# Kernel tuning notes

Measured on AMD Instinct MI355X. Metric: run time of the kernel, lower is better.

The kernel has to match this reference:

```python
import jax, jax.numpy as jnp
import numpy as np

N_FFT = 1024
HOP = 256
CACHE = N_FFT - 1  # causal left padding
EPS = 1e-12
BATCH = 16
SAMPLES = HOP * 2048


def _make_weight():
    # DFT basis modulated by a periodic Hann window (torch.hann_window default).
    n = np.arange(N_FFT, dtype=np.float32)
    k = np.arange(N_FFT // 2 + 1, dtype=np.float32)[:, None]
    ang = (-2.0 * np.pi / N_FFT) * k * n[None, :]
    win = 0.5 * (1.0 - np.cos(2.0 * np.pi * n / N_FFT))
    w = np.concatenate([np.cos(ang), np.sin(ang)], axis=0) * win  # [2*(N//2+1), N_FFT]
    return jnp.asarray(w, dtype=jnp.float32)[:, None, :]  # [O, I=1, K]


def setup_inputs() -> dict:
    key = jax.random.key(0)
    x = jax.random.normal(key, (BATCH, SAMPLES), dtype=jnp.float32)
    return {"x": x, "weight": _make_weight()}


def reference(x, weight):
    if x.ndim == 2:
        x = x[:, None, :]  # [B, 1, T]
    # causal constant (zero) padding on the left
    x = jnp.pad(x, ((0, 0), (0, 0), (CACHE, 0)))
    # strided conv against the fixed DFT basis: [B, 2*(N//2+1), L]
    y = jax.lax.conv_general_dilated(
        x, weight, window_strides=(HOP,), padding='VALID',
        dimension_numbers=('NCH', 'OIH', 'NCH'))
    B, C, T = y.shape
    y = y.reshape(B, 2, C // 2, T)  # real/imag split
    mag = jnp.sqrt(jnp.clip(jnp.sum(y * y, axis=1), EPS, None))  # [B, N//2+1, L]
    return mag
```

## Files before the change

### kernel.cpp

```cpp
#include <hip/hip_runtime.h>
#include <stdint.h>

#define SAMPLES   524288
#define BATCH     16
#define T_FRAMES  2048
#define K_FFT     1024
#define HOPSZ     256
#define CACHEPAD  1023
#define NCH       513
#define XROW      525312

typedef __bf16          bf16x8 __attribute__((ext_vector_type(8)));
typedef float           f32x4  __attribute__((ext_vector_type(4)));
typedef unsigned short  u16x8  __attribute__((ext_vector_type(8)));

__device__ __forceinline__ unsigned short f2bf(float f) {
    union { float f; unsigned u; } v; v.f = f;
    unsigned r = v.u + 0x7fffu + ((v.u >> 16) & 1u);
    return (unsigned short)(r >> 16);
}

__global__ void prep(const float* __restrict__ x, const float* __restrict__ wsrc,
                     unsigned short* __restrict__ Xb, unsigned short* __restrict__ Wb) {
    const int bid = blockIdx.x;
    const int tid = threadIdx.x;
    if (bid < 512) {
        int gid = bid * 256 + tid;
        int m   = gid >> 7;
        int kc  = (gid & 127) << 3;
        int q = m >> 5, h = (m >> 4) & 1, r = m & 15;
        int bin  = q * 16 + r;
        int srow = (h == 0) ? bin : (bin == 0 ? 512 : NCH + bin);
        const float* s = wsrc + (long long)srow * K_FFT + kc;
        f32x4 a = *(const f32x4*)s;
        f32x4 c = *(const f32x4*)(s + 4);
        union { u16x8 v; unsigned short e[8]; } o;
        o.e[0]=f2bf(a[0]); o.e[1]=f2bf(a[1]); o.e[2]=f2bf(a[2]); o.e[3]=f2bf(a[3]);
        o.e[4]=f2bf(c[0]); o.e[5]=f2bf(c[1]); o.e[6]=f2bf(c[2]); o.e[7]=f2bf(c[3]);
        *(u16x8*)(Wb + (long long)m * K_FFT + kc) = o.v;
    } else {
        int id  = bid - 512;
        int bat = id >> 8;
        int bx  = id & 255;
        unsigned short* xbo = Xb + (long long)bat * XROW;
        if (bx == 0) {
            for (int j = tid; j < CACHEPAD; j += 256) xbo[j] = 0;
            if (tid == 0) xbo[XROW - 1] = 0;
        }
        int i0 = (bx * 256 + tid) * 8;
        const float* xb = x + (long long)bat * SAMPLES;
        f32x4 a = *(const f32x4*)&xb[i0];
        f32x4 c = *(const f32x4*)&xb[i0 + 4];
        unsigned short* dst = xbo + CACHEPAD + i0;
        dst[0]=f2bf(a[0]); dst[1]=f2bf(a[1]); dst[2]=f2bf(a[2]); dst[3]=f2bf(a[3]);
        dst[4]=f2bf(c[0]); dst[5]=f2bf(c[1]); dst[6]=f2bf(c[2]); dst[7]=f2bf(c[3]);
    }
}

__device__ __forceinline__ void gll16(const unsigned short* g, unsigned short* s) {
    __builtin_amdgcn_global_load_lds(
        (const __attribute__((address_space(1))) void*)g,
        (__attribute__((address_space(3))) void*)s,
        16, 0, 0);
}

#define MFMA(a,b,c) __builtin_amdgcn_mfma_f32_16x16x32_bf16((a),(b),(c),0,0,0)

__global__ __launch_bounds__(512, 2)
void stft_gemm(const unsigned short* __restrict__ Xb,
               const unsigned short* __restrict__ Wb,
               float* __restrict__ out) {
    __shared__ unsigned short S[65536];

    const int id  = blockIdx.x;
    const int xcd = id & 7;
    const int u   = id >> 3;
    const int nt  = u >> 4;
    const int ft  = (xcd << 4) | (u & 15);
    const int b   = ft >> 3;
    const int t0  = (ft & 7) << 8;

    const int tid = threadIdx.x;
    const int l   = tid & 63;
    const int wv  = tid >> 6;
    const int ln  = l & 15;
    const int qd  = l >> 4;
    const int wm  = wv & 1;
    const int wn  = wv >> 1;

    const int sr0 = wv * 32 + (l >> 2);
    const int sr1 = sr0 + 16;
    const int sch = ((l & 3) ^ ((l >> 3) & 3)) * 8;
    const unsigned short* wA0 = Wb + (long long)(nt * 256 + sr0) * K_FFT + sch;
    const unsigned short* wA1 = Wb + (long long)(nt * 256 + sr1) * K_FFT + sch;
    const unsigned short* xbase = Xb + (long long)b * XROW;
    const unsigned short* fB0 = xbase + (t0 + sr0) * HOPSZ + sch;
    const unsigned short* fB1 = xbase + (t0 + sr1) * HOPSZ + sch;
    const int d0 = wv * 1024;
    const int d1 = d0 + 512;

    const int cx   = (qd ^ ((ln >> 1) & 3)) * 8;
    const int aoff = (wm * 128 + ln) * 32 + cx;
    const int boff = (wn * 64  + ln) * 32 + cx;

    f32x4 acc[8][4];
    #pragma unroll
    for (int i = 0; i < 8; ++i)
        #pragma unroll
        for (int jn = 0; jn < 4; ++jn) acc[i][jn] = (f32x4){0.f,0.f,0.f,0.f};

    gll16(wA0 +  0, S +     0 + d0);  gll16(wA1 +  0, S +     0 + d1);
    gll16(fB0 +  0, S +  8192 + d0);  gll16(fB1 +  0, S +  8192 + d1);
    gll16(wA0 + 32, S + 16384 + d0);  gll16(wA1 + 32, S + 16384 + d1);
    gll16(fB0 + 32, S + 24576 + d0);  gll16(fB1 + 32, S + 24576 + d1);
    gll16(wA0 + 64, S + 32768 + d0);  gll16(wA1 + 64, S + 32768 + d1);
    gll16(fB0 + 64, S + 40960 + d0);  gll16(fB1 + 64, S + 40960 + d1);
    asm volatile("s_waitcnt vmcnt(4)" ::: "memory");
    __builtin_amdgcn_s_barrier();

    #pragma unroll 1
    for (int j = 0; j < 16; ++j) {
        const int bb  = (j & 1) << 15;
        const int bb1 = bb ^ 32768;
        const int kA  = j * 64 + 96;
        const int kB  = j * 64 + 128;

        bf16x8 av[8];
        if (j < 15) { gll16(wA0 + kA, S + bb1 + 16384 + d0);
                      gll16(wA1 + kA, S + bb1 + 16384 + d1); }
        {
            const unsigned short* pA = S + bb + aoff;
            const unsigned short* pB = S + bb + 8192 + boff;
            #pragma unroll
            for (int i = 0; i < 8; ++i) av[i] = *(const bf16x8*)(pA + i * 512);
            bf16x8 b0 = *(const bf16x8*)(pB);
            bf16x8 b1 = *(const bf16x8*)(pB + 512);
            __builtin_amdgcn_s_barrier();
            __builtin_amdgcn_s_setprio(1);
            #pragma unroll
            for (int i = 0; i < 8; ++i) {
                acc[i][0] = MFMA(av[i], b0, acc[i][0]);
                acc[i][1] = MFMA(av[i], b1, acc[i][1]);
            }
            __builtin_amdgcn_s_setprio(0);
            __builtin_amdgcn_s_barrier();
        }
        if (j < 15) { gll16(fB0 + kA, S + bb1 + 24576 + d0);
                      gll16(fB1 + kA, S + bb1 + 24576 + d1); }
        {
            const unsigned short* pB = S + bb + 8192 + boff;
            bf16x8 b2 = *(const bf16x8*)(pB + 1024);
            bf16x8 b3 = *(const bf16x8*)(pB + 1536);
            __builtin_amdgcn_s_barrier();
            __builtin_amdgcn_s_setprio(1);
            #pragma unroll
            for (int i = 0; i < 8; ++i) {
                acc[i][2] = MFMA(av[i], b2, acc[i][2]);
                acc[i][3] = MFMA(av[i], b3, acc[i][3]);
            }
            __builtin_amdgcn_s_setprio(0);
            __builtin_amdgcn_s_barrier();
        }
        if (j < 14) { gll16(wA0 + kB, S + bb + d0);
                      gll16(wA1 + kB, S + bb + d1); }
        {
            const unsigned short* pA = S + bb + 16384 + aoff;
            const unsigned short* pB = S + bb + 24576 + boff;
            #pragma unroll
            for (int i = 0; i < 8; ++i) av[i] = *(const bf16x8*)(pA + i * 512);
            bf16x8 b0 = *(const bf16x8*)(pB);
            bf16x8 b1 = *(const bf16x8*)(pB + 512);
            __builtin_amdgcn_s_barrier();
            __builtin_amdgcn_s_setprio(1);
            #pragma unroll
            for (int i = 0; i < 8; ++i) {
                acc[i][0] = MFMA(av[i], b0, acc[i][0]);
                acc[i][1] = MFMA(av[i], b1, acc[i][1]);
            }
            __builtin_amdgcn_s_setprio(0);
            __builtin_amdgcn_s_barrier();
        }
        if (j < 14) { gll16(fB0 + kB, S + bb + 8192 + d0);
                      gll16(fB1 + kB, S + bb + 8192 + d1); }
        {
            const unsigned short* pB = S + bb + 24576 + boff;
            bf16x8 b2 = *(const bf16x8*)(pB + 1024);
            bf16x8 b3 = *(const bf16x8*)(pB + 1536);
            __builtin_amdgcn_s_barrier();
            __builtin_amdgcn_s_setprio(1);
            #pragma unroll
            for (int i = 0; i < 8; ++i) {
                acc[i][2] = MFMA(av[i], b2, acc[i][2]);
                acc[i][3] = MFMA(av[i], b3, acc[i][3]);
            }
            __builtin_amdgcn_s_setprio(0);
            if (j == 14) { asm volatile("s_waitcnt vmcnt(0)" ::: "memory"); }
            else         { asm volatile("s_waitcnt vmcnt(4)" ::: "memory"); }
            __builtin_amdgcn_s_barrier();
        }
    }

    float* outb = out + (long long)b * (NCH * T_FRAMES);
    const int tb = t0 + wn * 64 + ln;
    const int binbase = (nt * 8 + wm * 4) * 16 + qd * 4;
    #pragma unroll
    for (int p = 0; p < 4; ++p) {
        #pragma unroll
        for (int jn = 0; jn < 4; ++jn) {
            const int t = tb + jn * 16;
            #pragma unroll
            for (int r = 0; r < 4; ++r) {
                float re = acc[2 * p][jn][r];
                float im = acc[2 * p + 1][jn][r];
                int bin = binbase + p * 16 + r;
                if (bin == 0) {
                    outb[t] = sqrtf(fmaxf(re * re, 1e-12f));
                    outb[(long long)512 * T_FRAMES + t] = sqrtf(fmaxf(im * im, 1e-12f));
                } else {
                    outb[(long long)bin * T_FRAMES + t] =
                        sqrtf(fmaxf(re * re + im * im, 1e-12f));
                }
            }
        }
    }
}

extern "C" void kernel_launch(void* const* d_in, const int* in_sizes, int n_in,
                              void* d_out, int out_size, void* d_ws, size_t ws_size,
                              hipStream_t stream) {
    const float* x  = (const float*)d_in[0];
    const float* wt = (const float*)d_in[1];
    float* out = (float*)d_out;

    unsigned short* Xb = (unsigned short*)d_ws;
    unsigned short* Wb = (unsigned short*)((char*)d_ws + (size_t)33554432);

    prep<<<4608, 256, 0, stream>>>(x, wt, Xb, Wb);
    stft_gemm<<<512, 512, 0, stream>>>(Xb, Wb, out);
}
```

Measured before the change: 154.3 us.

## Process two frame tiles per block with continuous pipelined K loop

Each block now computes two consecutive 256-frame tiles for the same bin tile. The two K loops are merged into one 32-step double-buffered loop, so prefetch of the second tile starts before the first tile's epilogue. Accumulators are written out and cleared mid-loop. The grid drops from 512 to 256 blocks. The goal is to amortise pipeline ramp-up and drain and the block launch cost, but there are fewer blocks to fill the CUs and the epilogue now sits inside the main loop.

```diff
diff --git a/kernel.cpp b/kernel.cpp
--- a/kernel.cpp
+++ b/kernel.cpp
@@ -75,10 +75,10 @@
     const int id  = blockIdx.x;
     const int xcd = id & 7;
     const int u   = id >> 3;
-    const int nt  = u >> 4;
-    const int ft  = (xcd << 4) | (u & 15);
-    const int b   = ft >> 3;
-    const int t0  = (ft & 7) << 8;
+    const int nt  = u >> 3;
+    const int fp  = (xcd << 3) | (u & 7);
+    const int b   = fp >> 2;
+    const int offF = (fp & 3) << 9;
 
     const int tid = threadIdx.x;
     const int l   = tid & 63;
@@ -94,8 +94,8 @@
     const unsigned short* wA0 = Wb + (long long)(nt * 256 + sr0) * K_FFT + sch;
     const unsigned short* wA1 = Wb + (long long)(nt * 256 + sr1) * K_FFT + sch;
     const unsigned short* xbase = Xb + (long long)b * XROW;
-    const unsigned short* fB0 = xbase + (t0 + sr0) * HOPSZ + sch;
-    const unsigned short* fB1 = xbase + (t0 + sr1) * HOPSZ + sch;
+    const unsigned short* fB0 = xbase + (offF + sr0) * HOPSZ + sch;
+    const unsigned short* fB1 = xbase + (offF + sr1) * HOPSZ + sch;
     const int d0 = wv * 1024;
     const int d1 = d0 + 512;
 
@@ -118,15 +118,22 @@
     asm volatile("s_waitcnt vmcnt(4)" ::: "memory");
     __builtin_amdgcn_s_barrier();
 
+    float* outb = out + (long long)b * (NCH * T_FRAMES);
+    const int binbase = (nt * 8 + wm * 4) * 16 + qd * 4;
+
     #pragma unroll 1
-    for (int j = 0; j < 16; ++j) {
+    for (int j = 0; j < 32; ++j) {
         const int bb  = (j & 1) << 15;
         const int bb1 = bb ^ 32768;
-        const int kA  = j * 64 + 96;
-        const int kB  = j * 64 + 128;
+        const int s1  = j + 1;
+        const int s2  = j + 2;
+        const int kA  = ((s1 & 15) << 6) + 32;
+        const int kB  = (s2 & 15) << 6;
+        const int ho1 = (s1 & 16) << 12;
+        const int ho2 = (s2 & 16) << 12;
 
         bf16x8 av[8];
-        if (j < 15) { gll16(wA0 + kA, S + bb1 + 16384 + d0);
+        if (j < 31) { gll16(wA0 + kA, S + bb1 + 16384 + d0);
                       gll16(wA1 + kA, S + bb1 + 16384 + d1); }
         {
             const unsigned short* pA = S + bb + aoff;
@@ -145,8 +152,8 @@
             __builtin_amdgcn_s_setprio(0);
             __builtin_amdgcn_s_barrier();
         }
-        if (j < 15) { gll16(fB0 + kA, S + bb1 + 24576 + d0);
-                      gll16(fB1 + kA, S + bb1 + 24576 + d1); }
+        if (j < 31) { gll16(fB0 + ho1 + kA, S + bb1 + 24576 + d0);
+                      gll16(fB1 + ho1 + kA, S + bb1 + 24576 + d1); }
         {
             const unsigned short* pB = S + bb + 8192 + boff;
             bf16x8 b2 = *(const bf16x8*)(pB + 1024);
@@ -161,7 +168,7 @@
             __builtin_amdgcn_s_setprio(0);
             __builtin_amdgcn_s_barrier();
         }
-        if (j < 14) { gll16(wA0 + kB, S + bb + d0);
+        if (j < 30) { gll16(wA0 + kB, S + bb + d0);
                       gll16(wA1 + kB, S + bb + d1); }
         {
             const unsigned short* pA = S + bb + 16384 + aoff;
@@ -180,8 +187,8 @@
             __builtin_amdgcn_s_setprio(0);
             __builtin_amdgcn_s_barrier();
         }
-        if (j < 14) { gll16(fB0 + kB, S + bb + 8192 + d0);
-                      gll16(fB1 + kB, S + bb + 8192 + d1); }
+        if (j < 30) { gll16(fB0 + ho2 + kB, S + bb + 8192 + d0);
+                      gll16(fB1 + ho2 + kB, S + bb + 8192 + d1); }
         {
             const unsigned short* pB = S + bb + 24576 + boff;
             bf16x8 b2 = *(const bf16x8*)(pB + 1024);
@@ -194,31 +201,59 @@
                 acc[i][3] = MFMA(av[i], b3, acc[i][3]);
             }
             __builtin_amdgcn_s_setprio(0);
-            if (j == 14) { asm volatile("s_waitcnt vmcnt(0)" ::: "memory"); }
+            if (j == 30) { asm volatile("s_waitcnt vmcnt(0)" ::: "memory"); }
             else         { asm volatile("s_waitcnt vmcnt(4)" ::: "memory"); }
             __builtin_amdgcn_s_barrier();
         }
+
+        if (j == 15) {
+            const int tb = offF + wn * 64 + ln;
+            #pragma unroll
+            for (int p = 0; p < 4; ++p) {
+                #pragma unroll
+                for (int jn = 0; jn < 4; ++jn) {
+                    const int t = tb + jn * 16;
+                    #pragma unroll
+                    for (int r = 0; r < 4; ++r) {
+                        float re = acc[2 * p][jn][r];
+                        float im = acc[2 * p + 1][jn][r];
+                        int bin = binbase + p * 16 + r;
+                        if (bin == 0) {
+                            outb[t] = sqrtf(fmaxf(re * re, 1e-12f));
+                            outb[(long long)512 * T_FRAMES + t] = sqrtf(fmaxf(im * im, 1e-12f));
+                        } else {
+                            outb[(long long)bin * T_FRAMES + t] =
+                                sqrtf(fmaxf(re * re + im * im, 1e-12f));
+                        }
+                    }
+                }
+            }
+            #pragma unroll
+            for (int i = 0; i < 8; ++i)
+                #pragma unroll
+                for (int jn = 0; jn < 4; ++jn) acc[i][jn] = (f32x4){0.f,0.f,0.f,0.f};
+        }
     }
 
-    float* outb = out + (long long)b * (NCH * T_FRAMES);
-    const int tb = t0 + wn * 64 + ln;
-    const int binbase = (nt * 8 + wm * 4) * 16 + qd * 4;
-    #pragma unroll
-    for (int p = 0; p < 4; ++p) {
+    {
+        const int tb = offF + 256 + wn * 64 + ln;
         #pragma unroll
-        for (int jn = 0; jn < 4; ++jn) {
-            const int t = tb + jn * 16;
-            #pragma unroll
-            for (int r = 0; r < 4; ++r) {
-                float re = acc[2 * p][jn][r];
-                float im = acc[2 * p + 1][jn][r];
-                int bin = binbase + p * 16 + r;
-                if (bin == 0) {
-                    outb[t] = sqrtf(fmaxf(re * re, 1e-12f));
-                    outb[(long long)512 * T_FRAMES + t] = sqrtf(fmaxf(im * im, 1e-12f));
-                } else {
-                    outb[(long long)bin * T_FRAMES + t] =
-                        sqrtf(fmaxf(re * re + im * im, 1e-12f));
+        for (int p = 0; p < 4; ++p) {
+            #pragma unroll
+            for (int jn = 0; jn < 4; ++jn) {
+                const int t = tb + jn * 16;
+                #pragma unroll
+                for (int r = 0; r < 4; ++r) {
+                    float re = acc[2 * p][jn][r];
+                    float im = acc[2 * p + 1][jn][r];
+                    int bin = binbase + p * 16 + r;
+                    if (bin == 0) {
+                        outb[t] = sqrtf(fmaxf(re * re, 1e-12f));
+                        outb[(long long)512 * T_FRAMES + t] = sqrtf(fmaxf(im * im, 1e-12f));
+                    } else {
+                        outb[(long long)bin * T_FRAMES + t] =
+                            sqrtf(fmaxf(re * re + im * im, 1e-12f));
+                    }
                 }
             }
         }
@@ -236,5 +271,5 @@
     unsigned short* Wb = (unsigned short*)((char*)d_ws + (size_t)33554432);
 
     prep<<<4608, 256, 0, stream>>>(x, wt, Xb, Wb);
-    stft_gemm<<<512, 512, 0, stream>>>(Xb, Wb, out);
-}
+    stft_gemm<<<256, 512, 0, stream>>>(Xb, Wb, out);
+}
```

Measured after the change: 153.1 us. No clear change (-0.8%).
